# Kernel tuning notes

Hardware: AMD Instinct MI355X
Metric: run time of the kernel (lower is better)

## Reference

```python
import jax, jax.numpy as jnp
import numpy as np

N_PIX = 196608  # 12 * 128**2 (HEALPix nside=128)
F = 32          # filters (Fin == Fout for residual)
DM = 2          # depth multiplier


def _cheb_sep_conv(x, idx, wnb, wd, wp, b):
    """Separable Chebyshev graph conv.
    x: [B,N,F] maps; idx: [N,nb] neighbor indices; wnb: [N,nb] Laplacian weights;
    wd: [K,F,DM] depthwise Chebyshev weights; wp: [F*DM,Fout] pointwise; b: [Fout].
    """
    def L(t):  # sparse Laplacian apply via fixed-degree neighbor gather
        return jnp.einsum('bnjf,nj->bnf', t[:, idx, :], wnb)
    K = wd.shape[0]
    Ts = [x, L(x)]
    for _ in range(K - 2):  # Chebyshev recursion T_k = 2 L T_{k-1} - T_{k-2}
        Ts.append(2.0 * L(Ts[-1]) - Ts[-2])
    T = jnp.stack(Ts, 0)                      # [K,B,N,F]
    y = jnp.einsum('kbnf,kfd->bnfd', T, wd)   # depthwise over Chebyshev orders
    Bb, Nn, Ff, Dd = y.shape
    y = y.reshape(Bb, Nn, Ff * Dd)
    return y @ wp + b                         # pointwise mix to Fout


def _layernorm(x, gamma, beta, eps=1e-6):
    mu = jnp.mean(x, axis=-1, keepdims=True)
    var = jnp.mean(jnp.square(x - mu), axis=-1, keepdims=True)
    return (x - mu) * jax.lax.rsqrt(var + eps) * gamma + beta


def setup_inputs() -> dict:
    key = jax.random.key(0)
    ks = jax.random.split(key, 10)
    inp = {
        'maps': jax.random.normal(ks[0], (1, N_PIX, F), jnp.float32),
        'idx1': jax.random.randint(ks[1], (N_PIX, 8), 0, N_PIX, jnp.int32),
        'w1_nb': jax.random.normal(ks[2], (N_PIX, 8), jnp.float32) * 0.1,
        'idx2': jax.random.randint(ks[3], (N_PIX, 20), 0, N_PIX, jnp.int32),
        'w2_nb': jax.random.normal(ks[4], (N_PIX, 20), jnp.float32) * 0.1,
        'wd1': jax.random.normal(ks[5], (6, F, DM), jnp.float32) * 0.1,
        'wp1': jax.random.normal(ks[6], (F * DM, F), jnp.float32) * 0.1,
        'b1': jnp.zeros((F,), jnp.float32),
        'gamma1': jnp.ones((F,), jnp.float32),
        'beta1': jnp.zeros((F,), jnp.float32),
        'wd2': jax.random.normal(ks[7], (10, F, DM), jnp.float32) * 0.1,
        'wp2': jax.random.normal(ks[8], (F * DM, F), jnp.float32) * 0.1,
        'b2': jnp.zeros((F,), jnp.float32),
        'gamma2': jnp.ones((F,), jnp.float32),
        'beta2': jnp.zeros((F,), jnp.float32),
    }
    return inp


def reference(maps, idx1, w1_nb, idx2, w2_nb, wd1, wp1, b1, gamma1, beta1,
              wd2, wp2, b2, gamma2, beta2):
    res = maps
    x = _cheb_sep_conv(maps, idx1, w1_nb, wd1, wp1, b1)   # K=6, nb=8
    x = jax.nn.relu(x)
    x = _layernorm(x, gamma1, beta1)
    x = _cheb_sep_conv(x, idx2, w2_nb, wd2, wp2, b2)      # K=10, nb=20
    x = jax.nn.relu(x)
    x = _layernorm(x, gamma2, beta2)
    return x + res
```

## Files before the change

kernel.cpp:

```cpp
#include <hip/hip_runtime.h>

constexpr int NPIX = 196608;
constexpr int FF   = 32;
constexpr size_t SLOT = (size_t)NPIX * FF;

typedef short bf16x8 __attribute__((ext_vector_type(8)));
typedef float f32x4  __attribute__((ext_vector_type(4)));
typedef int   i32x4  __attribute__((ext_vector_type(4)));
typedef uint  u32x4  __attribute__((ext_vector_type(4)));

__device__ __forceinline__ float blo(uint u) {
    union { float f; uint i; } v; v.i = u << 16; return v.f;
}
__device__ __forceinline__ float bhi(uint u) {
    union { float f; uint i; } v; v.i = u & 0xffff0000u; return v.f;
}
__device__ __forceinline__ ushort f2b(float f) {
    union { float f; uint i; } v; v.f = f;
    uint r = v.i + 0x7fffu + ((v.i >> 16) & 1u);
    return (ushort)(r >> 16);
}
__device__ __forceinline__ uint pack2(float lo, float hi) {
    return ((uint)f2b(hi) << 16) | (uint)f2b(lo);
}

__global__ __launch_bounds__(256) void f2b_kernel(const float* __restrict__ src,
                                                  ushort* __restrict__ dst) {
    int i = (blockIdx.x * 256 + threadIdx.x) * 4;
    f32x4 v = *reinterpret_cast<const f32x4*>(src + i);
    ushort4 o;
    o.x = f2b(v.x); o.y = f2b(v.y); o.z = f2b(v.z); o.w = f2b(v.w);
    *reinterpret_cast<ushort4*>(dst + i) = o;
}

template<int NB>
__global__ __launch_bounds__(256) void sort_edges(
    const int*   __restrict__ idx,
    const float* __restrict__ wnb,
    ulong*       __restrict__ edges)
{
    int n = blockIdx.x * 256 + threadIdx.x;
    ulong a[NB];
#pragma unroll
    for (int j = 0; j < NB; ++j) {
        union { float f; uint u; } w; w.f = wnb[(size_t)n * NB + j];
        a[j] = ((ulong)(uint)idx[(size_t)n * NB + j] << 32) | (ulong)w.u;
    }
#pragma unroll
    for (int r = 0; r < NB; ++r) {
#pragma unroll
        for (int i = (r & 1); i + 1 < NB; i += 2) {
            if (a[i] > a[i + 1]) { ulong t = a[i]; a[i] = a[i + 1]; a[i + 1] = t; }
        }
    }
#pragma unroll
    for (int j = 0; j < NB; ++j)
        edges[(size_t)n * NB + j] = a[j];
}

template<int NB, int NCH, bool INIT>
__global__ __launch_bounds__(256, 4) void cheb_stepC(
    const ushort* __restrict__ Tprev,
    const ushort* __restrict__ Told,
    ushort*       __restrict__ Tout,
    const ulong*  __restrict__ edges)
{
    constexpr int CH = NB / NCH;
    int t = blockIdx.x * 256 + threadIdx.x;
    int n = t >> 2;
    int h = t & 3;

    ulong E[NB];
    const ulong* ep = edges + (size_t)n * NB;
#pragma unroll
    for (int j = 0; j < NB; ++j) E[j] = ep[j];

    const u32x4* Tp = reinterpret_cast<const u32x4*>(Tprev);
    float s0 = 0.f, s1 = 0.f, s2 = 0.f, s3 = 0.f;
    float s4 = 0.f, s5 = 0.f, s6 = 0.f, s7 = 0.f;

#pragma unroll
    for (int c = 0; c < NCH; ++c) {
        u32x4 u[CH];
        float w[CH];
#pragma unroll
        for (int i = 0; i < CH; ++i) {
            ulong e = E[c * CH + i];
            union { float f; uint u; } wv; wv.u = (uint)e;
            w[i] = wv.f;
            u[i] = Tp[(size_t)(int)(e >> 32) * 4 + h];
        }
#pragma unroll
        for (int i = 0; i < CH; ++i) {
            s0 += w[i] * blo(u[i].x); s1 += w[i] * bhi(u[i].x);
            s2 += w[i] * blo(u[i].y); s3 += w[i] * bhi(u[i].y);
            s4 += w[i] * blo(u[i].z); s5 += w[i] * bhi(u[i].z);
            s6 += w[i] * blo(u[i].w); s7 += w[i] * bhi(u[i].w);
        }
        __builtin_amdgcn_sched_barrier(0);
    }

    size_t base = (size_t)n * 4 + h;
    u32x4 o;
    if (INIT) {
        o.x = pack2(s0, s1); o.y = pack2(s2, s3);
        o.z = pack2(s4, s5); o.w = pack2(s6, s7);
    } else {
        u32x4 told = reinterpret_cast<const u32x4*>(Told)[base];
        o.x = pack2(2.f * s0 - blo(told.x), 2.f * s1 - bhi(told.x));
        o.y = pack2(2.f * s2 - blo(told.y), 2.f * s3 - bhi(told.y));
        o.z = pack2(2.f * s4 - blo(told.z), 2.f * s5 - bhi(told.z));
        o.w = pack2(2.f * s6 - blo(told.w), 2.f * s7 - bhi(told.w));
    }
    reinterpret_cast<u32x4*>(Tout)[base] = o;
}

template<int NB, bool INIT>
__global__ __launch_bounds__(256, 4) void cheb_step4(
    const ushort* __restrict__ Tprev,
    const ushort* __restrict__ Told,
    ushort*       __restrict__ Tout,
    const int*    __restrict__ idx,
    const float*  __restrict__ wnb)
{
    int t = blockIdx.x * 256 + threadIdx.x;
    int n = t >> 2;
    int h = t & 3;

    const i32x4* ip = reinterpret_cast<const i32x4*>(idx + (size_t)n * NB);
    const f32x4* wv = reinterpret_cast<const f32x4*>(wnb + (size_t)n * NB);
    i32x4 I[NB / 4];
    f32x4 W[NB / 4];
#pragma unroll
    for (int j = 0; j < NB / 4; ++j) { I[j] = ip[j]; W[j] = wv[j]; }

    const u32x4* Tp = reinterpret_cast<const u32x4*>(Tprev);
    float s0 = 0.f, s1 = 0.f, s2 = 0.f, s3 = 0.f;
    float s4 = 0.f, s5 = 0.f, s6 = 0.f, s7 = 0.f;

#pragma unroll
    for (int j = 0; j < NB / 4; ++j) {
        i32x4 i4 = I[j]; f32x4 w4 = W[j];
#pragma unroll
        for (int e = 0; e < 4; ++e) {
            int   ii = (e == 0) ? i4.x : (e == 1) ? i4.y : (e == 2) ? i4.z : i4.w;
            float ww = (e == 0) ? w4.x : (e == 1) ? w4.y : (e == 2) ? w4.z : w4.w;
            u32x4 u = Tp[(size_t)ii * 4 + h];
            s0 += ww * blo(u.x); s1 += ww * bhi(u.x);
            s2 += ww * blo(u.y); s3 += ww * bhi(u.y);
            s4 += ww * blo(u.z); s5 += ww * bhi(u.z);
            s6 += ww * blo(u.w); s7 += ww * bhi(u.w);
        }
    }

    size_t base = (size_t)n * 4 + h;
    u32x4 o;
    if (INIT) {
        o.x = pack2(s0, s1); o.y = pack2(s2, s3);
        o.z = pack2(s4, s5); o.w = pack2(s6, s7);
    } else {
        u32x4 told = reinterpret_cast<const u32x4*>(Told)[base];
        o.x = pack2(2.f * s0 - blo(told.x), 2.f * s1 - bhi(told.x));
        o.y = pack2(2.f * s2 - blo(told.y), 2.f * s3 - bhi(told.y));
        o.z = pack2(2.f * s4 - blo(told.z), 2.f * s5 - bhi(told.z));
        o.w = pack2(2.f * s6 - blo(told.w), 2.f * s7 - bhi(told.w));
    }
    reinterpret_cast<u32x4*>(Tout)[base] = o;
}

template<int K, bool RESIDUAL, bool OUT_BF16>
__global__ __launch_bounds__(256, 4) void finish_gemm(
    const ushort* __restrict__ chain,
    const float*  __restrict__ wd,
    const float*  __restrict__ wp,
    const float*  __restrict__ bias,
    const float*  __restrict__ gamma,
    const float*  __restrict__ beta,
    const float*  __restrict__ resid,
    void*         __restrict__ outp)
{
    constexpr int KW = K * 32;
    constexpr int WSTRIDE = KW + 8;
    __shared__ float swp[64 * 33];
    __shared__ __align__(16) ushort sW[32][WSTRIDE];

    int tid = threadIdx.x;
    int wv = tid >> 6, l = tid & 63;
    int r = l & 15, hi = l >> 4;
    int nbase = blockIdx.x * 64 + wv * 16;

    bf16x8 aF[K];
#pragma unroll
    for (int k = 0; k < K; ++k)
        aF[k] = *reinterpret_cast<const bf16x8*>(
            chain + (size_t)k * SLOT + (size_t)(nbase + r) * FF + hi * 8);

    for (int i = tid; i < 64 * 32; i += 256) {
        int u = i >> 5, g = i & 31;
        swp[u * 33 + g] = wp[i];
    }
    __syncthreads();

    for (int i = tid; i < 32 * KW; i += 256) {
        int g = i / KW, kf = i - g * KW;
        int f = kf & 31;
        float2 wdv = *reinterpret_cast<const float2*>(wd + (size_t)kf * 2);
        float w2 = wdv.x * swp[(2 * f) * 33 + g] + wdv.y * swp[(2 * f + 1) * 33 + g];
        sW[g][kf] = f2b(w2);
    }
    __syncthreads();

    f32x4 acc0 = {0.f, 0.f, 0.f, 0.f};
    f32x4 acc1 = {0.f, 0.f, 0.f, 0.f};
#pragma unroll
    for (int k = 0; k < K; ++k) {
        bf16x8 b0 = *reinterpret_cast<const bf16x8*>(&sW[r][k * 32 + hi * 8]);
        bf16x8 b1 = *reinterpret_cast<const bf16x8*>(&sW[16 + r][k * 32 + hi * 8]);
        acc0 = __builtin_amdgcn_mfma_f32_16x16x32_bf16(aF[k], b0, acc0, 0, 0, 0);
        acc1 = __builtin_amdgcn_mfma_f32_16x16x32_bf16(aF[k], b1, acc1, 0, 0, 0);
    }

    float bias_lo = bias[r],  bias_hi = bias[16 + r];
    float gam_lo  = gamma[r], gam_hi  = gamma[16 + r];
    float bet_lo  = beta[r],  bet_hi  = beta[16 + r];

#pragma unroll
    for (int v = 0; v < 4; ++v) {
        acc0[v] = fmaxf(acc0[v] + bias_lo, 0.f);
        acc1[v] = fmaxf(acc1[v] + bias_hi, 0.f);
    }
#pragma unroll
    for (int v = 0; v < 4; ++v) {
        float s1 = acc0[v] + acc1[v];
        float s2 = acc0[v] * acc0[v] + acc1[v] * acc1[v];
#pragma unroll
        for (int m = 1; m < 16; m <<= 1) {
            s1 += __shfl_xor(s1, m);
            s2 += __shfl_xor(s2, m);
        }
        float mu  = s1 * (1.f / 32.f);
        float var = s2 * (1.f / 32.f) - mu * mu;
        float rs  = rsqrtf(var + 1e-6f);
        int n = nbase + hi * 4 + v;
        size_t o0 = (size_t)n * FF + r;
        size_t o1 = o0 + 16;
        float z0 = (acc0[v] - mu) * rs * gam_lo + bet_lo;
        float z1 = (acc1[v] - mu) * rs * gam_hi + bet_hi;
        if (RESIDUAL) { z0 += resid[o0]; z1 += resid[o1]; }
        if (OUT_BF16) {
            ((ushort*)outp)[o0] = f2b(z0);
            ((ushort*)outp)[o1] = f2b(z1);
        } else {
            ((float*)outp)[o0] = z0;
            ((float*)outp)[o1] = z1;
        }
    }
}

extern "C" void kernel_launch(void* const* d_in, const int* in_sizes, int n_in,
                              void* d_out, int out_size, void* d_ws, size_t ws_size,
                              hipStream_t stream) {
    const float* maps = (const float*)d_in[0];
    const int*   idx1 = (const int*)  d_in[1];
    const float* w1nb = (const float*)d_in[2];
    const int*   idx2 = (const int*)  d_in[3];
    const float* w2nb = (const float*)d_in[4];
    const float* wd1  = (const float*)d_in[5];
    const float* wp1  = (const float*)d_in[6];
    const float* b1   = (const float*)d_in[7];
    const float* g1   = (const float*)d_in[8];
    const float* be1  = (const float*)d_in[9];
    const float* wd2  = (const float*)d_in[10];
    const float* wp2  = (const float*)d_in[11];
    const float* b2   = (const float*)d_in[12];
    const float* g2   = (const float*)d_in[13];
    const float* be2  = (const float*)d_in[14];
    float* out = (float*)d_out;

    ushort* slots = (ushort*)d_ws;
    ushort* B = slots;
    ushort* A = slots + 4 * SLOT;
    ulong* edges2 = (ulong*)(slots + 10 * SLOT);
    ulong* edges1 = edges2 + (size_t)NPIX * 20;

    const size_t needSorted = 10 * SLOT * 2 + (size_t)NPIX * 20 * 8 + (size_t)NPIX * 8 * 8;
    const bool useSorted = ws_size >= needSorted;

    const int stepBlocks = NPIX * 4 / 256;
    const int cvtBlocks  = NPIX * FF / (256 * 4);
    const int finBlocks  = NPIX / 64;
    const int sortBlocks = NPIX / 256;

    if (useSorted) {
        sort_edges<8><<<sortBlocks, 256, 0, stream>>>(idx1, w1nb, edges1);
        sort_edges<20><<<sortBlocks, 256, 0, stream>>>(idx2, w2nb, edges2);
    }

    f2b_kernel<<<cvtBlocks, 256, 0, stream>>>(maps, A);
    if (useSorted) {
        cheb_stepC<8, 2, true><<<stepBlocks, 256, 0, stream>>>(A, nullptr, A + SLOT, edges1);
        cheb_stepC<8, 2, false><<<stepBlocks, 256, 0, stream>>>(A + SLOT,     A,            A + 2 * SLOT, edges1);
        cheb_stepC<8, 2, false><<<stepBlocks, 256, 0, stream>>>(A + 2 * SLOT, A + SLOT,     A + 3 * SLOT, edges1);
        cheb_stepC<8, 2, false><<<stepBlocks, 256, 0, stream>>>(A + 3 * SLOT, A + 2 * SLOT, A + 4 * SLOT, edges1);
        cheb_stepC<8, 2, false><<<stepBlocks, 256, 0, stream>>>(A + 4 * SLOT, A + 3 * SLOT, A + 5 * SLOT, edges1);
    } else {
        cheb_step4<8, true><<<stepBlocks, 256, 0, stream>>>(A, nullptr, A + SLOT, idx1, w1nb);
        cheb_step4<8, false><<<stepBlocks, 256, 0, stream>>>(A + SLOT,     A,            A + 2 * SLOT, idx1, w1nb);
        cheb_step4<8, false><<<stepBlocks, 256, 0, stream>>>(A + 2 * SLOT, A + SLOT,     A + 3 * SLOT, idx1, w1nb);
        cheb_step4<8, false><<<stepBlocks, 256, 0, stream>>>(A + 3 * SLOT, A + 2 * SLOT, A + 4 * SLOT, idx1, w1nb);
        cheb_step4<8, false><<<stepBlocks, 256, 0, stream>>>(A + 4 * SLOT, A + 3 * SLOT, A + 5 * SLOT, idx1, w1nb);
    }
    finish_gemm<6, false, true><<<finBlocks, 256, 0, stream>>>(A, wd1, wp1, b1, g1, be1, nullptr, B);

    if (useSorted) {
        cheb_stepC<20, 5, true><<<stepBlocks, 256, 0, stream>>>(B, nullptr, B + SLOT, edges2);
        for (int k = 2; k <= 9; ++k)
            cheb_stepC<20, 5, false><<<stepBlocks, 256, 0, stream>>>(
                B + (size_t)(k - 1) * SLOT, B + (size_t)(k - 2) * SLOT,
                B + (size_t)k * SLOT, edges2);
    } else {
        cheb_step4<20, true><<<stepBlocks, 256, 0, stream>>>(B, nullptr, B + SLOT, idx2, w2nb);
        for (int k = 2; k <= 9; ++k)
            cheb_step4<20, false><<<stepBlocks, 256, 0, stream>>>(
                B + (size_t)(k - 1) * SLOT, B + (size_t)(k - 2) * SLOT,
                B + (size_t)k * SLOT, idx2, w2nb);
    }
    finish_gemm<10, true, false><<<finBlocks, 256, 0, stream>>>(B, wd2, wp2, b2, g2, be2, maps, out);
}
```

Measured before the change: 761.2 us.

## Pad 20-neighbor edge lists into bucketed 32-slot layout for aligned gathers

Builds a padded 32-slot edge list per pixel for the second conv. Each neighbor is placed into a slot bucket keyed by its source-index range, so that at each slot position the lanes of a wave tend to gather from nearby memory regions. Empty slots get zero weight and repeat the last source index. The new step kernel loads edges as ulong2 pairs and prefetches the next chunk. The cost is 60% more gather and FMA work (32 vs 20 slots) and a larger edge buffer, with edges1 moved into spare B slot space, in exchange for better gather locality across lanes.

Result: slower. 1.464 ms (+92.3%).

```diff
diff --git a/kernel.cpp b/kernel.cpp
--- a/kernel.cpp
+++ b/kernel.cpp
@@ -22,6 +22,9 @@
 }
 __device__ __forceinline__ uint pack2(float lo, float hi) {
     return ((uint)f2b(hi) << 16) | (uint)f2b(lo);
+}
+__device__ __forceinline__ float wbits(ulong e) {
+    union { float f; uint u; } v; v.u = (uint)e; return v.f;
 }
 
 __global__ __launch_bounds__(256) void f2b_kernel(const float* __restrict__ src,
@@ -58,6 +61,126 @@
         edges[(size_t)n * NB + j] = a[j];
 }
 
+template<int NB, int NSLOT>
+__global__ __launch_bounds__(256) void build_slots(
+    const int*   __restrict__ idx,
+    const float* __restrict__ wnb,
+    ulong*       __restrict__ edgesP)
+{
+    constexpr int NBUCK = NSLOT / 4;
+    constexpr int BW = NPIX / NBUCK;
+    int n = blockIdx.x * 256 + threadIdx.x;
+
+    ulong a[NB];
+#pragma unroll
+    for (int j = 0; j < NB; ++j) {
+        union { float f; uint u; } w; w.f = wnb[(size_t)n * NB + j];
+        a[j] = ((ulong)(uint)idx[(size_t)n * NB + j] << 32) | (ulong)w.u;
+    }
+#pragma unroll
+    for (int r = 0; r < NB; ++r) {
+#pragma unroll
+        for (int i = (r & 1); i + 1 < NB; i += 2) {
+            if (a[i] > a[i + 1]) { ulong t = a[i]; a[i] = a[i + 1]; a[i + 1] = t; }
+        }
+    }
+
+    int s[NB];
+    int prev = -1;
+#pragma unroll
+    for (int j = 0; j < NB; ++j) {
+        int src = (int)(a[j] >> 32);
+        int b = src / BW;
+        int want = b * 4;
+        s[j] = (prev + 1 > want) ? prev + 1 : want;
+        prev = s[j];
+    }
+    if (s[NB - 1] > NSLOT - 1) s[NB - 1] = NSLOT - 1;
+#pragma unroll
+    for (int j = NB - 2; j >= 0; --j)
+        if (s[j] > s[j + 1] - 1) s[j] = s[j + 1] - 1;
+
+    ulong* base = edgesP + (size_t)n * NSLOT;
+#pragma unroll
+    for (int t = 0; t < NSLOT; ++t)
+        base[t] = 0xFFFFFFFF00000000ull;
+#pragma unroll
+    for (int j = 0; j < NB; ++j)
+        base[s[j]] = a[j];
+    uint lastSrc = (uint)(a[0] >> 32);
+#pragma unroll
+    for (int t = 0; t < NSLOT; ++t) {
+        ulong e = base[t];
+        if ((uint)(e >> 32) == 0xFFFFFFFFu) base[t] = ((ulong)lastSrc << 32);
+        else lastSrc = (uint)(e >> 32);
+    }
+}
+
+template<int NSLOT, bool INIT>
+__global__ __launch_bounds__(256, 4) void cheb_stepP(
+    const ushort* __restrict__ Tprev,
+    const ushort* __restrict__ Told,
+    ushort*       __restrict__ Tout,
+    const ulong*  __restrict__ edgesP)
+{
+    constexpr int NCH = NSLOT / 4;
+    int t = blockIdx.x * 256 + threadIdx.x;
+    int n = t >> 2;
+    int h = t & 3;
+
+    const ulong2* ep = reinterpret_cast<const ulong2*>(edgesP + (size_t)n * NSLOT);
+    const u32x4*  Tp = reinterpret_cast<const u32x4*>(Tprev);
+    size_t base = (size_t)n * 4 + h;
+
+    u32x4 told;
+    if (!INIT) told = reinterpret_cast<const u32x4*>(Told)[base];
+
+    float s0 = 0.f, s1 = 0.f, s2 = 0.f, s3 = 0.f;
+    float s4 = 0.f, s5 = 0.f, s6 = 0.f, s7 = 0.f;
+
+    ulong2 e01 = ep[0], e23 = ep[1];
+
+#pragma unroll
+    for (int c = 0; c < NCH; ++c) {
+        ulong E0 = e01.x, E1 = e01.y, E2 = e23.x, E3 = e23.y;
+        u32x4 u0 = Tp[(size_t)(uint)(E0 >> 32) * 4 + h];
+        u32x4 u1 = Tp[(size_t)(uint)(E1 >> 32) * 4 + h];
+        u32x4 u2 = Tp[(size_t)(uint)(E2 >> 32) * 4 + h];
+        u32x4 u3 = Tp[(size_t)(uint)(E3 >> 32) * 4 + h];
+        if (c + 1 < NCH) { e01 = ep[2 * (c + 1)]; e23 = ep[2 * (c + 1) + 1]; }
+        float w0 = wbits(E0), w1 = wbits(E1), w2 = wbits(E2), w3 = wbits(E3);
+        s0 += w0 * blo(u0.x); s1 += w0 * bhi(u0.x);
+        s2 += w0 * blo(u0.y); s3 += w0 * bhi(u0.y);
+        s4 += w0 * blo(u0.z); s5 += w0 * bhi(u0.z);
+        s6 += w0 * blo(u0.w); s7 += w0 * bhi(u0.w);
+        s0 += w1 * blo(u1.x); s1 += w1 * bhi(u1.x);
+        s2 += w1 * blo(u1.y); s3 += w1 * bhi(u1.y);
+        s4 += w1 * blo(u1.z); s5 += w1 * bhi(u1.z);
+        s6 += w1 * blo(u1.w); s7 += w1 * bhi(u1.w);
+        s0 += w2 * blo(u2.x); s1 += w2 * bhi(u2.x);
+        s2 += w2 * blo(u2.y); s3 += w2 * bhi(u2.y);
+        s4 += w2 * blo(u2.z); s5 += w2 * bhi(u2.z);
+        s6 += w2 * blo(u2.w); s7 += w2 * bhi(u2.w);
+        s0 += w3 * blo(u3.x); s1 += w3 * bhi(u3.x);
+        s2 += w3 * blo(u3.y); s3 += w3 * bhi(u3.y);
+        s4 += w3 * blo(u3.z); s5 += w3 * bhi(u3.z);
+        s6 += w3 * blo(u3.w); s7 += w3 * bhi(u3.w);
+        __builtin_amdgcn_sched_barrier(0);
+    }
+
+    u32x4 o;
+    if (INIT) {
+        o.x = pack2(s0, s1); o.y = pack2(s2, s3);
+        o.z = pack2(s4, s5); o.w = pack2(s6, s7);
+    } else {
+        o.x = pack2(2.f * s0 - blo(told.x), 2.f * s1 - bhi(told.x));
+        o.y = pack2(2.f * s2 - blo(told.y), 2.f * s3 - bhi(told.y));
+        o.z = pack2(2.f * s4 - blo(told.z), 2.f * s5 - bhi(told.z));
+        o.w = pack2(2.f * s6 - blo(told.w), 2.f * s7 - bhi(told.w));
+    }
+    reinterpret_cast<u32x4*>(Tout)[base] = o;
+}
+
 template<int NB, int NCH, bool INIT>
 __global__ __launch_bounds__(256, 4) void cheb_stepC(
     const ushort* __restrict__ Tprev,
@@ -86,9 +209,8 @@
 #pragma unroll
         for (int i = 0; i < CH; ++i) {
             ulong e = E[c * CH + i];
-            union { float f; uint u; } wv; wv.u = (uint)e;
-            w[i] = wv.f;
-            u[i] = Tp[(size_t)(int)(e >> 32) * 4 + h];
+            w[i] = wbits(e);
+            u[i] = Tp[(size_t)(uint)(e >> 32) * 4 + h];
         }
 #pragma unroll
         for (int i = 0; i < CH; ++i) {
@@ -280,11 +402,11 @@
     ushort* slots = (ushort*)d_ws;
     ushort* B = slots;
     ushort* A = slots + 4 * SLOT;
-    ulong* edges2 = (ulong*)(slots + 10 * SLOT);
-    ulong* edges1 = edges2 + (size_t)NPIX * 20;
-
-    const size_t needSorted = 10 * SLOT * 2 + (size_t)NPIX * 20 * 8 + (size_t)NPIX * 8 * 8;
-    const bool useSorted = ws_size >= needSorted;
+    ulong* edges1  = (ulong*)(B + SLOT);
+    ulong* edgesP2 = (ulong*)(slots + 10 * SLOT);
+
+    const size_t needFull = 10 * SLOT * 2 + (size_t)NPIX * 32 * 8;
+    const bool useSorted = ws_size >= needFull;
 
     const int stepBlocks = NPIX * 4 / 256;
     const int cvtBlocks  = NPIX * FF / (256 * 4);
@@ -293,32 +415,29 @@
 
     if (useSorted) {
         sort_edges<8><<<sortBlocks, 256, 0, stream>>>(idx1, w1nb, edges1);
-        sort_edges<20><<<sortBlocks, 256, 0, stream>>>(idx2, w2nb, edges2);
-    }
-
-    f2b_kernel<<<cvtBlocks, 256, 0, stream>>>(maps, A);
-    if (useSorted) {
+        build_slots<20, 32><<<sortBlocks, 256, 0, stream>>>(idx2, w2nb, edgesP2);
+
+        f2b_kernel<<<cvtBlocks, 256, 0, stream>>>(maps, A);
         cheb_stepC<8, 2, true><<<stepBlocks, 256, 0, stream>>>(A, nullptr, A + SLOT, edges1);
         cheb_stepC<8, 2, false><<<stepBlocks, 256, 0, stream>>>(A + SLOT,     A,            A + 2 * SLOT, edges1);
         cheb_stepC<8, 2, false><<<stepBlocks, 256, 0, stream>>>(A + 2 * SLOT, A + SLOT,     A + 3 * SLOT, edges1);
         cheb_stepC<8, 2, false><<<stepBlocks, 256, 0, stream>>>(A + 3 * SLOT, A + 2 * SLOT, A + 4 * SLOT, edges1);
         cheb_stepC<8, 2, false><<<stepBlocks, 256, 0, stream>>>(A + 4 * SLOT, A + 3 * SLOT, A + 5 * SLOT, edges1);
+        finish_gemm<6, false, true><<<finBlocks, 256, 0, stream>>>(A, wd1, wp1, b1, g1, be1, nullptr, B);
+
+        cheb_stepP<32, true><<<stepBlocks, 256, 0, stream>>>(B, nullptr, B + SLOT, edgesP2);
+        for (int k = 2; k <= 9; ++k)
+            cheb_stepP<32, false><<<stepBlocks, 256, 0, stream>>>(
+                B + (size_t)(k - 1) * SLOT, B + (size_t)(k - 2) * SLOT,
+                B + (size_t)k * SLOT, edgesP2);
     } else {
+        f2b_kernel<<<cvtBlocks, 256, 0, stream>>>(maps, A);
         cheb_step4<8, true><<<stepBlocks, 256, 0, stream>>>(A, nullptr, A + SLOT, idx1, w1nb);
         cheb_step4<8, false><<<stepBlocks, 256, 0, stream>>>(A + SLOT,     A,            A + 2 * SLOT, idx1, w1nb);
         cheb_step4<8, false><<<stepBlocks, 256, 0, stream>>>(A + 2 * SLOT, A + SLOT,     A + 3 * SLOT, idx1, w1nb);
         cheb_step4<8, false><<<stepBlocks, 256, 0, stream>>>(A + 3 * SLOT, A + 2 * SLOT, A + 4 * SLOT, idx1, w1nb);
         cheb_step4<8, false><<<stepBlocks, 256, 0, stream>>>(A + 4 * SLOT, A + 3 * SLOT, A + 5 * SLOT, idx1, w1nb);
-    }
-    finish_gemm<6, false, true><<<finBlocks, 256, 0, stream>>>(A, wd1, wp1, b1, g1, be1, nullptr, B);
-
-    if (useSorted) {
-        cheb_stepC<20, 5, true><<<stepBlocks, 256, 0, stream>>>(B, nullptr, B + SLOT, edges2);
-        for (int k = 2; k <= 9; ++k)
-            cheb_stepC<20, 5, false><<<stepBlocks, 256, 0, stream>>>(
-                B + (size_t)(k - 1) * SLOT, B + (size_t)(k - 2) * SLOT,
-                B + (size_t)k * SLOT, edges2);
-    } else {
+        finish_gemm<6, false, true><<<finBlocks, 256, 0, stream>>>(A, wd1, wp1, b1, g1, be1, nullptr, B);
         cheb_step4<20, true><<<stepBlocks, 256, 0, stream>>>(B, nullptr, B + SLOT, idx2, w2nb);
         for (int k = 2; k <= 9; ++k)
             cheb_step4<20, false><<<stepBlocks, 256, 0, stream>>>(
```
